# Kernel optimization log

Hardware: AMD Instinct MI355X
Metric: run time of the kernel (lower is better)

## Reference

```python
import jax, jax.numpy as jnp
import numpy as np

BINS = 30
MMT = 0.75
LOSS_WEIGHT = 1.0
N, C = 2000000, 16


def setup_inputs() -> dict:
    key = jax.random.key(0)
    k1, k2 = jax.random.split(key)
    pred = jax.random.normal(k1, (N, C), dtype=jnp.float32)
    target = jax.random.randint(k2, (N, C), 0, 2, dtype=jnp.int32)
    acc_sum = jnp.zeros((BINS,), dtype=jnp.float32)
    return {"pred": pred, "target": target, "acc_sum": acc_sum}


def reference(pred, target, acc_sum):
    t = target.astype(pred.dtype)
    tot = float(pred.size)

    # gradient density g = |sigmoid(pred) - target|, detached
    g = jnp.abs(jax.nn.sigmoid(jax.lax.stop_gradient(pred)) - t)

    # edges are i/BINS, last edge bumped by 1e-6 => bin = floor(g*BINS), clipped
    idx = jnp.clip((g * BINS).astype(jnp.int32), 0, BINS - 1)  # [N, C]

    flat_idx = idx.reshape(-1)
    counts = jax.ops.segment_sum(
        jnp.ones_like(flat_idx, dtype=pred.dtype), flat_idx, num_segments=BINS
    )  # [BINS]

    nonempty = counts > 0
    new_acc = jnp.where(nonempty, MMT * acc_sum + (1.0 - MMT) * counts, acc_sum)
    safe_acc = jnp.where(nonempty, new_acc, jnp.ones_like(new_acc))

    n = jnp.maximum(jnp.sum(nonempty).astype(pred.dtype), 1.0)
    per_bin_w = tot / safe_acc / n  # [BINS]
    weights = jax.lax.stop_gradient(per_bin_w[idx])  # [N, C]

    # stable BCE with logits: t*softplus(-x) + (1-t)*softplus(x)
    bce = t * jax.nn.softplus(-pred) + (1.0 - t) * jax.nn.softplus(pred)
    loss = jnp.sum(bce * weights) / tot
    return loss * LOSS_WEIGHT
```

## Files before the change

kernel.cpp:

```cpp
#include <hip/hip_runtime.h>

#define BINS 30
#define MMT 0.75f
#define LOSS_WEIGHT 1.0f

#define RSTRIDE 31
#define NTHREADS 256
#define HWORDS (NTHREADS * RSTRIDE)
#define CNT_ONE (1u << 20)
#define SUM_MASK 0xFFFFFu
#define SSCALE 256.0f
#define INV_SSCALE (1.0f / 256.0f)


__global__ __launch_bounds__(256) void ghmc_pass1(
                           const float4* __restrict__ pred4,
                           const int4*   __restrict__ tgt4,
                           float*        __restrict__ gS,
                           unsigned int* __restrict__ gC,
                           unsigned int* __restrict__ gDone,
                           const float*  __restrict__ acc_sum,
                           float*        __restrict__ out,
                           int nvec, int total, float tot) {
    __shared__ unsigned int sH[HWORDS];
    __shared__ unsigned int sPs[4 * BINS];
    __shared__ unsigned int sPc[4 * BINS];
    __shared__ unsigned int sLast;
    const int t = threadIdx.x;

    for (int k = t; k < HWORDS; k += NTHREADS) sH[k] = 0u;
    __syncthreads();

    unsigned int* const row = &sH[t * RSTRIDE];

    const int stride = gridDim.x * blockDim.x;
    for (int i = blockIdx.x * blockDim.x + t; i < nvec; i += stride) {
        float4 p  = pred4[i];
        int4   tv = tgt4[i];
        #pragma unroll
        for (int j = 0; j < 4; ++j) {
            float x  = (&p.x)[j];
            int   tt = (&tv.x)[j];
            float z = tt ? -x : x;
            float a = __expf(-fabsf(z));
            float h = 1.0f + a;
            float r = __builtin_amdgcn_rcpf(h);
            float g = (z >= 0.0f) ? r : 1.0f - r;
            float sp = fmaxf(z, 0.0f) + __logf(h);
            int b = (int)(g * 30.0f);
            b = b > (BINS - 1) ? (BINS - 1) : b;
            b = b < 0 ? 0 : b;
            unsigned int v = (unsigned int)(sp * SSCALE + 0.5f) + CNT_ONE;
            row[b] += v;
        }
    }

    if (blockIdx.x == 0 && t == 0) {
        const float* predf = (const float*)pred4;
        const int*   tgtf  = (const int*)tgt4;
        for (int e = nvec * 4; e < total; ++e) {
            float x  = predf[e];
            int   tt = tgtf[e];
            float z = tt ? -x : x;
            float a = __expf(-fabsf(z));
            float h = 1.0f + a;
            float r = __builtin_amdgcn_rcpf(h);
            float g = (z >= 0.0f) ? r : 1.0f - r;
            float sp = fmaxf(z, 0.0f) + __logf(h);
            int b = (int)(g * 30.0f);
            b = b > (BINS - 1) ? (BINS - 1) : b;
            b = b < 0 ? 0 : b;
            row[b] += (unsigned int)(sp * SSCALE + 0.5f) + CNT_ONE;
        }
    }
    __syncthreads();

    {
        const int w = t >> 6;
        const int l = t & 63;
        if (l < BINS) {
            unsigned int cs = 0u, ss = 0u;
            const int r0 = w * 64;
            #pragma unroll 8
            for (int r2 = 0; r2 < 64; ++r2) {
                unsigned int v = sH[(r0 + r2) * RSTRIDE + l];
                cs += v >> 20;
                ss += v & SUM_MASK;
            }
            sPs[w * BINS + l] = ss;
            sPc[w * BINS + l] = cs;
        }
    }
    __syncthreads();

    if (t < BINS) {
        unsigned int cs = 0u, ss = 0u;
        #pragma unroll
        for (int w = 0; w < 4; ++w) {
            ss += sPs[w * BINS + t];
            cs += sPc[w * BINS + t];
        }
        if (cs != 0u) {
            atomicAdd(&gS[t], (float)ss * INV_SSCALE);
            atomicAdd(&gC[t], cs);
        }
        __threadfence();
    }
    __syncthreads();

    if (t == 0) sLast = (atomicAdd(gDone, 1u) == (unsigned int)(gridDim.x - 1)) ? 1u : 0u;
    __syncthreads();
    if (sLast && t < 64) {
        unsigned int c = 0u; float s = 0.0f;
        if (t < BINS) {
            c = atomicAdd(&gC[t], 0u);
            s = atomicAdd(&gS[t], 0.0f);
        }
        unsigned long long m = __ballot(t < BINS && c != 0u);
        float nf = fmaxf((float)__popcll(m), 1.0f);
        float term = 0.0f;
        if (t < BINS && c != 0u) {
            float na = MMT * acc_sum[t] + (1.0f - MMT) * (float)c;
            term = (tot / na / nf) * s;
        }
        float loss = 0.0f;
        for (int b = 0; b < BINS; ++b) loss += __shfl(term, b);
        if (t == 0) out[0] = (loss / tot) * LOSS_WEIGHT;
    }
}

extern "C" void kernel_launch(void* const* d_in, const int* in_sizes, int n_in,
                              void* d_out, int out_size, void* d_ws, size_t ws_size,
                              hipStream_t stream) {
    const float* pred    = (const float*)d_in[0];
    const int*   target  = (const int*)d_in[1];
    const float* acc_sum = (const float*)d_in[2];

    const int total = in_sizes[0];
    const int nvec  = total / 4;

    float*        gS    = (float*)d_ws;
    unsigned int* gC    = (unsigned int*)((char*)d_ws + 256);
    unsigned int* gDone = (unsigned int*)((char*)d_ws + 512);

    hipMemsetAsync(d_ws, 0, 768, stream);

    const int blocks = 1024;
    ghmc_pass1<<<blocks, NTHREADS, 0, stream>>>(
        (const float4*)pred, (const int4*)target, gS, gC, gDone, acc_sum,
        (float*)d_out, nvec, total, (float)total);
}
```

Measured before the change: 305.1 us.

## Split histogram pass into two launches with strided and contiguous block partitioning

The input is split in half and handled by two back-to-back launches of the same kernel. The first launch keeps the grid-stride access pattern and the second gives each block a contiguous chunk. A shared completion counter across both launches (totalBlocks) decides which block does the final reduction. This looks like an experiment in access locality, and it adds a second launch plus an extra histogram flush and atomic merge per block.

Measured after the change: 332.8 us. 1.09x slower.

```diff
diff --git a/kernel.cpp b/kernel.cpp
--- a/kernel.cpp
+++ b/kernel.cpp
@@ -13,6 +13,19 @@
 #define INV_SSCALE (1.0f / 256.0f)
 
 
+__device__ __forceinline__ void ghm_elem(float x, int tt, unsigned int* __restrict__ row) {
+    float z = tt ? -x : x;
+    float a = __expf(-fabsf(z));
+    float h = 1.0f + a;
+    float r = __builtin_amdgcn_rcpf(h);
+    float g = (z >= 0.0f) ? r : 1.0f - r;
+    float sp = fmaxf(z, 0.0f) + __logf(h);
+    int b = (int)(g * 30.0f);
+    b = b > (BINS - 1) ? (BINS - 1) : b;
+    b = b < 0 ? 0 : b;
+    row[b] += (unsigned int)(sp * SSCALE + 0.5f) + CNT_ONE;
+}
+
 __global__ __launch_bounds__(256) void ghmc_pass1(
                            const float4* __restrict__ pred4,
                            const int4*   __restrict__ tgt4,
@@ -21,7 +34,8 @@
                            unsigned int* __restrict__ gDone,
                            const float*  __restrict__ acc_sum,
                            float*        __restrict__ out,
-                           int nvec, int total, float tot) {
+                           int gbase, int ngroups, int contig,
+                           int totalBlocks, int do_tail, int total, float tot) {
     __shared__ unsigned int sH[HWORDS];
     __shared__ unsigned int sPs[4 * BINS];
     __shared__ unsigned int sPc[4 * BINS];
@@ -33,45 +47,38 @@
 
     unsigned int* const row = &sH[t * RSTRIDE];
 
-    const int stride = gridDim.x * blockDim.x;
-    for (int i = blockIdx.x * blockDim.x + t; i < nvec; i += stride) {
-        float4 p  = pred4[i];
-        int4   tv = tgt4[i];
-        #pragma unroll
-        for (int j = 0; j < 4; ++j) {
-            float x  = (&p.x)[j];
-            int   tt = (&tv.x)[j];
-            float z = tt ? -x : x;
-            float a = __expf(-fabsf(z));
-            float h = 1.0f + a;
-            float r = __builtin_amdgcn_rcpf(h);
-            float g = (z >= 0.0f) ? r : 1.0f - r;
-            float sp = fmaxf(z, 0.0f) + __logf(h);
-            int b = (int)(g * 30.0f);
-            b = b > (BINS - 1) ? (BINS - 1) : b;
-            b = b < 0 ? 0 : b;
-            unsigned int v = (unsigned int)(sp * SSCALE + 0.5f) + CNT_ONE;
-            row[b] += v;
+    if (contig) {
+        const int perBlock = (ngroups + gridDim.x - 1) / gridDim.x;
+        const int b0  = blockIdx.x * perBlock;
+        int rem = ngroups - b0;
+        const int lim = (rem < perBlock) ? rem : perBlock;
+        for (int i = t; i < lim; i += NTHREADS) {
+            const int g = gbase + b0 + i;
+            float4 p  = pred4[g];
+            int4   tv = tgt4[g];
+            ghm_elem(p.x, tv.x, row);
+            ghm_elem(p.y, tv.y, row);
+            ghm_elem(p.z, tv.z, row);
+            ghm_elem(p.w, tv.w, row);
+        }
+    } else {
+        const int stride = gridDim.x * blockDim.x;
+        for (int i = blockIdx.x * blockDim.x + t; i < ngroups; i += stride) {
+            const int g = gbase + i;
+            float4 p  = pred4[g];
+            int4   tv = tgt4[g];
+            ghm_elem(p.x, tv.x, row);
+            ghm_elem(p.y, tv.y, row);
+            ghm_elem(p.z, tv.z, row);
+            ghm_elem(p.w, tv.w, row);
         }
     }
 
-    if (blockIdx.x == 0 && t == 0) {
+    if (do_tail && blockIdx.x == 0 && t == 0) {
         const float* predf = (const float*)pred4;
         const int*   tgtf  = (const int*)tgt4;
-        for (int e = nvec * 4; e < total; ++e) {
-            float x  = predf[e];
-            int   tt = tgtf[e];
-            float z = tt ? -x : x;
-            float a = __expf(-fabsf(z));
-            float h = 1.0f + a;
-            float r = __builtin_amdgcn_rcpf(h);
-            float g = (z >= 0.0f) ? r : 1.0f - r;
-            float sp = fmaxf(z, 0.0f) + __logf(h);
-            int b = (int)(g * 30.0f);
-            b = b > (BINS - 1) ? (BINS - 1) : b;
-            b = b < 0 ? 0 : b;
-            row[b] += (unsigned int)(sp * SSCALE + 0.5f) + CNT_ONE;
-        }
+        for (int e = (total / 4) * 4; e < total; ++e)
+            ghm_elem(predf[e], tgtf[e], row);
     }
     __syncthreads();
 
@@ -108,7 +115,7 @@
     }
     __syncthreads();
 
-    if (t == 0) sLast = (atomicAdd(gDone, 1u) == (unsigned int)(gridDim.x - 1)) ? 1u : 0u;
+    if (t == 0) sLast = (atomicAdd(gDone, 1u) == (unsigned int)(totalBlocks - 1)) ? 1u : 0u;
     __syncthreads();
     if (sLast && t < 64) {
         unsigned int c = 0u; float s = 0.0f;
@@ -137,7 +144,9 @@
     const float* acc_sum = (const float*)d_in[2];
 
     const int total = in_sizes[0];
-    const int nvec  = total / 4;
+    const int groupsTotal = total / 4;
+    const int gA = groupsTotal / 2;
+    const int gB = groupsTotal - gA;
 
     float*        gS    = (float*)d_ws;
     unsigned int* gC    = (unsigned int*)((char*)d_ws + 256);
@@ -146,7 +155,15 @@
     hipMemsetAsync(d_ws, 0, 768, stream);
 
     const int blocks = 1024;
+    const int totalBlocks = 2 * blocks;
+
     ghmc_pass1<<<blocks, NTHREADS, 0, stream>>>(
         (const float4*)pred, (const int4*)target, gS, gC, gDone, acc_sum,
-        (float*)d_out, nvec, total, (float)total);
+        (float*)d_out, 0, gA, 0, totalBlocks, 0,
+        total, (float)total);
+
+    ghmc_pass1<<<blocks, NTHREADS, 0, stream>>>(
+        (const float4*)pred, (const int4*)target, gS, gC, gDone, acc_sum,
+        (float*)d_out, gA, gB, 1, totalBlocks, 1,
+        total, (float)total);
 }
```
